# Kernel tuning notes

Measured on AMD Instinct MI355X. Metric: run time of the kernel, lower is better.

## Reference

```python
import jax, jax.numpy as jnp
import numpy as np

# Dimensions (match init_kwargs / input_specs)
NF, NLOC, NALL = 1, 1024, 2048
N_DIM, E_DIM, A_DIM = 128, 16, 64
NNEI, A_SEL, AXIS = 120, 20, 4

act = jax.nn.silu


def _lin(key, i, o):
    k1, k2 = jax.random.split(key)
    w = jax.random.normal(k1, (i, o), jnp.float32) / np.float32(np.sqrt(i))
    b = jax.random.normal(k2, (o,), jnp.float32) * 0.01
    return w, b


def setup_inputs() -> dict:
    key = jax.random.key(0)
    ks = jax.random.split(key, 16)
    d = {}
    d["node_ebd_ext"] = jax.random.normal(ks[0], (NF, NALL, N_DIM), jnp.float32)
    d["edge_ebd"] = jax.random.normal(ks[1], (NF, NLOC, NNEI, E_DIM), jnp.float32)
    d["h2"] = jax.random.normal(ks[2], (NF, NLOC, NNEI, 3), jnp.float32)
    d["angle_ebd"] = jax.random.normal(ks[3], (NF, NLOC, A_SEL, A_SEL, A_DIM), jnp.float32)
    d["sw"] = jax.random.uniform(ks[4], (NF, NLOC, NNEI), jnp.float32)
    d["a_sw"] = jax.random.uniform(ks[5], (NF, NLOC, A_SEL), jnp.float32)
    d["nlist"] = jax.random.randint(ks[6], (NF, NLOC, NNEI), 0, NALL)
    d["nlist_mask"] = jnp.ones((NF, NLOC, NNEI), bool)
    d["a_nlist_mask"] = jnp.ones((NF, NLOC, A_SEL), bool)
    edge_info_dim = 2 * N_DIM + E_DIM          # 272
    angle_dim = A_DIM + N_DIM + 2 * E_DIM      # 224 (a_compress_rate == 0)
    d["w_node_self"], d["b_node_self"] = _lin(ks[7], N_DIM, N_DIM)
    d["w_node_sym"], d["b_node_sym"] = _lin(ks[8], (N_DIM + E_DIM) * AXIS, N_DIM)
    d["w_node_edge"], d["b_node_edge"] = _lin(ks[9], edge_info_dim, N_DIM)
    d["w_edge_self"], d["b_edge_self"] = _lin(ks[10], edge_info_dim, E_DIM)
    d["w_ea1"], d["b_ea1"] = _lin(ks[11], angle_dim, E_DIM)
    d["w_ea2"], d["b_ea2"] = _lin(ks[12], E_DIM, E_DIM)
    d["w_angle_self"], d["b_angle_self"] = _lin(ks[13], angle_dim, A_DIM)
    # res_residual update style: one learnable residual scale per update branch,
    # init 'const' with update_residual = 0.1
    d["n_res"] = jnp.full((3, N_DIM), 0.1, jnp.float32)  # self, sym, edge-message
    d["e_res"] = jnp.full((2, E_DIM), 0.1, jnp.float32)  # self, angle-message
    d["a_res"] = jnp.full((1, A_DIM), 0.1, jnp.float32)  # self
    return d


def _forward(node_ebd_ext, edge_ebd, h2, angle_ebd, sw, a_sw,
             w_node_self, b_node_self, w_node_sym, b_node_sym,
             w_node_edge, b_node_edge, w_edge_self, b_edge_self,
             w_ea1, b_ea1, w_ea2, b_ea2, w_angle_self, b_angle_self,
             n_res, e_res, a_res, nlist, nlist_mask, a_nlist_mask):
    nf, nall, n_dim = node_ebd_ext.shape
    _, nloc, nnei, e_dim = edge_ebd.shape
    a_sel = angle_ebd.shape[2]
    node_ebd = node_ebd_ext[:, :nloc]

    # gather neighbor node embeddings: nf x nloc x nnei x n_dim
    nei_node = jax.vmap(lambda tbl, idx: tbl[idx])(node_ebd_ext, nlist)
    nei_node = jnp.where(nlist_mask[..., None], nei_node, 0.0)

    # 1) node self update
    node_self_update = act(node_ebd @ w_node_self + b_node_self)

    # 2) node symmetrization update (grrg over both edge and neighbor-node features)
    wgt = (sw * nlist_mask)[..., None]

    def sym(ebd):
        e = ebd * wgt
        hg = jnp.einsum('flni,flnd->flid', h2, e) / np.float32(nnei)  # f,l,3,d
        grrg = jnp.einsum('flid,flia->flda', hg, hg[..., :AXIS]) / np.float32(3.0)
        return grrg.reshape(nf, nloc, -1)

    node_sym_in = jnp.concatenate([sym(nei_node), sym(edge_ebd)], axis=-1)
    node_sym_update = act(node_sym_in @ w_node_sym + b_node_sym)

    # 3) edge info = [node_i, node_j, edge_ij]
    node_i = jnp.broadcast_to(node_ebd[:, :, None, :], (nf, nloc, nnei, n_dim))
    edge_info = jnp.concatenate([node_i, nei_node, edge_ebd], axis=-1)

    # 3a) node <- edge message (sw-weighted mean over neighbors)
    node_edge_update = act(edge_info @ w_node_edge + b_node_edge) * sw[..., None]
    node_edge_update = node_edge_update.sum(axis=-2) / np.float32(nnei)

    node_new = (node_ebd + n_res[0] * node_self_update
                + n_res[1] * node_sym_update + n_res[2] * node_edge_update)

    # 4) edge self update
    edge_self_update = act(edge_info @ w_edge_self + b_edge_self)

    # 5) angle branch (a_compress_rate == 0)
    edge_for_angle = jnp.where(a_nlist_mask[..., None], edge_ebd[:, :, :a_sel, :], 0.0)
    node_angle = jnp.broadcast_to(node_ebd[:, :, None, None, :], (nf, nloc, a_sel, a_sel, n_dim))
    e_ik = jnp.broadcast_to(edge_for_angle[:, :, :, None, :], (nf, nloc, a_sel, a_sel, e_dim))
    e_ij = jnp.broadcast_to(edge_for_angle[:, :, None, :, :], (nf, nloc, a_sel, a_sel, e_dim))
    angle_info = jnp.concatenate([angle_ebd, node_angle, e_ik, e_ij], axis=-1)

    # edge <- angle message: sw-weighted reduce over one angle axis
    ea = act(angle_info @ w_ea1 + b_ea1)  # nf,nloc,a_sel,a_sel,e_dim
    weighted = a_sw[:, :, :, None, None] * a_sw[:, :, None, :, None] * ea
    reduced = weighted.sum(axis=-2) / np.float32(np.sqrt(a_sel))  # nf,nloc,a_sel,e_dim
    pad = jnp.zeros((nf, nloc, nnei - a_sel, e_dim), edge_ebd.dtype)
    padded = jnp.concatenate([reduced, pad], axis=2)
    full_mask = jnp.concatenate(
        [a_nlist_mask, jnp.zeros((nf, nloc, nnei - a_sel), bool)], axis=-1)
    # smooth_edge_update = False: keep original edge ebd where angle mask is off
    padded = jnp.where(full_mask[..., None], padded, edge_ebd)
    edge_angle_update = act(padded @ w_ea2 + b_ea2)

    edge_new = edge_ebd + e_res[0] * edge_self_update + e_res[1] * edge_angle_update

    # angle self update
    angle_self_update = act(angle_info @ w_angle_self + b_angle_self)
    angle_new = angle_ebd + a_res[0] * angle_self_update

    return node_new, edge_new, angle_new


def reference(node_ebd_ext, edge_ebd, h2, angle_ebd, sw, a_sw, nlist, nlist_mask,
              a_nlist_mask, w_node_self, b_node_self, w_node_sym, b_node_sym,
              w_node_edge, b_node_edge, w_edge_self, b_edge_self, w_ea1, b_ea1,
              w_ea2, b_ea2, w_angle_self, b_angle_self, n_res, e_res, a_res):
    return _forward(node_ebd_ext, edge_ebd, h2, angle_ebd, sw, a_sw,
                    w_node_self, b_node_self, w_node_sym, b_node_sym,
                    w_node_edge, b_node_edge, w_edge_self, b_edge_self,
                    w_ea1, b_ea1, w_ea2, b_ea2, w_angle_self, b_angle_self,
                    n_res, e_res, a_res, nlist, nlist_mask, a_nlist_mask)
```

## Files before the change

### kernel.cpp

```cpp
#include <hip/hip_runtime.h>
#include <math.h>

#define NLOC 1024
#define NALL 2048
#define NDIM 128
#define EDIM 16
#define ADIM 64
#define NNEI 120
#define ASEL 20


__device__ __forceinline__ float silu(float x) { return x / (1.f + __expf(-x)); }

__device__ __forceinline__ unsigned short f2bf(float f) {
    unsigned int u = __float_as_uint(f);
    u += 0x7fffu + ((u >> 16) & 1u);
    return (unsigned short)(u >> 16);
}

typedef __attribute__((ext_vector_type(8))) short bf16x8;
typedef __attribute__((ext_vector_type(4))) float f32x4;

__global__ __launch_bounds__(256) void k_prep(
    const float* __restrict__ node_ext,
    const float* __restrict__ w_ne, const float* __restrict__ b_ne,
    const float* __restrict__ w_es, const float* __restrict__ b_es,
    const float* __restrict__ w_ea1, const float* __restrict__ b_ea1,
    const float* __restrict__ w_as, const float* __restrict__ b_as,
    float* __restrict__ proj, float* __restrict__ pre_e,
    float* __restrict__ pre_a, unsigned short* __restrict__ wtb)
{
    const int b = blockIdx.x, t = threadIdx.x;
    if (b == 3072) {
        for (int idx = t; idx < 64 * 80; idx += 256) {
            int k = idx / 80, o = idx - k * 80;
            float v = (o < 16) ? w_ea1[k * 16 + o] : w_as[k * 64 + (o - 16)];
            wtb[o * 64 + k] = f2bf(v);
        }
        return;
    }
    __shared__ float x[128];
    const int row = (b < 2048) ? b : (b - 2048);
    if (t < 128) x[t] = node_ext[row * 128 + t];
    __syncthreads();
    if (b < 2048) {
        if (t < 144) {
            float acc = 0.f;
            if (t < 128) {
                for (int k = 0; k < 128; k++) acc += x[k] * w_ne[(128 + k) * 128 + t];
            } else {
                int o = t - 128;
                for (int k = 0; k < 128; k++) acc += x[k] * w_es[(128 + k) * 16 + o];
            }
            proj[b * 144 + t] = acc;
        }
    } else {
        int i = b - 2048;
        if (t < 144) {
            float acc;
            if (t < 128) {
                acc = b_ne[t];
                for (int k = 0; k < 128; k++) acc += x[k] * w_ne[k * 128 + t];
            } else {
                int o = t - 128;
                acc = b_es[o];
                for (int k = 0; k < 128; k++) acc += x[k] * w_es[k * 16 + o];
            }
            pre_e[i * 144 + t] = acc;
        } else if (t < 224) {
            int o = t - 144;
            float acc;
            if (o < 16) {
                acc = b_ea1[o];
                for (int k = 0; k < 128; k++) acc += x[k] * w_ea1[(64 + k) * 16 + o];
            } else {
                int o2 = o - 16;
                acc = b_as[o2];
                for (int k = 0; k < 128; k++) acc += x[k] * w_as[(64 + k) * 64 + o2];
            }
            pre_a[i * 80 + o] = acc;
        }
    }
}

__global__ __launch_bounds__(256) void k_angle(
    const float* __restrict__ angle, const float* __restrict__ edge,
    const float* __restrict__ asw,
    const float* __restrict__ w_ea1, const float* __restrict__ w_as,
    const unsigned short* __restrict__ wtb, const float* __restrict__ pre_a,
    const float* __restrict__ a_res,
    float* __restrict__ out_angle, float* __restrict__ reduced)
{
    const int i = blockIdx.x, t = threadIdx.x;
    const int lane = t & 63, wv = t >> 6;
    const int m = lane & 15, q = lane >> 4;

    __shared__ float eca_s[ASEL * 80], ecb_s[ASEL * 80], edge20_s[ASEL * EDIM];
    __shared__ float asw_s[ASEL], ares_s[ADIM], red_s[ASEL * 16];
    __shared__ unsigned short wt_s[80 * 72];

    for (int idx = t; idx < ASEL * EDIM; idx += 256)
        edge20_s[idx] = edge[(size_t)i * NNEI * EDIM + idx];
    if (t < ASEL) asw_s[t] = asw[i * ASEL + t];
    if (t < ADIM) ares_s[t] = a_res[t];
    for (int idx = t; idx < ASEL * 16; idx += 256) red_s[idx] = 0.f;
    for (int idx = t; idx < 80 * 64; idx += 256) {
        int o = idx >> 6, k = idx & 63;
        wt_s[o * 72 + k] = wtb[idx];
    }
    __syncthreads();

    bf16x8 bfrag[5][2];
    #pragma unroll
    for (int nt = 0; nt < 5; nt++)
        #pragma unroll
        for (int ks = 0; ks < 2; ks++)
            bfrag[nt][ks] = *(const bf16x8*)&wt_s[(nt * 16 + m) * 72 + ks * 32 + q * 8];

    for (int idx = t; idx < 2 * ASEL * 80; idx += 256) {
        int half = idx / 1600, rem = idx - half * 1600;
        int aa = rem / 80, o = rem - aa * 80;
        float acc = (half == 0) ? pre_a[i * 80 + o] : 0.f;
        if (o < 16) {
            const float* w = w_ea1 + (192 + half * 16) * 16 + o;
            #pragma unroll
            for (int k = 0; k < 16; k++) acc += edge20_s[aa * 16 + k] * w[k * 16];
        } else {
            const float* w = w_as + (192 + half * 16) * 64 + (o - 16);
            #pragma unroll
            for (int k = 0; k < 16; k++) acc += edge20_s[aa * 16 + k] * w[k * 64];
        }
        if (half == 0) eca_s[rem] = acc; else ecb_s[rem] = acc;
    }
    __syncthreads();

    for (int mt = wv; mt < 25; mt += 4) {
        const float* Arow = angle + ((size_t)i * 400 + mt * 16 + m) * 64 + q * 8;
        float4 x0 = *(const float4*)(Arow + 0);
        float4 x1 = *(const float4*)(Arow + 4);
        float4 x2 = *(const float4*)(Arow + 32);
        float4 x3 = *(const float4*)(Arow + 36);
        bf16x8 af0, af1;
        af0[0] = (short)f2bf(x0.x); af0[1] = (short)f2bf(x0.y);
        af0[2] = (short)f2bf(x0.z); af0[3] = (short)f2bf(x0.w);
        af0[4] = (short)f2bf(x1.x); af0[5] = (short)f2bf(x1.y);
        af0[6] = (short)f2bf(x1.z); af0[7] = (short)f2bf(x1.w);
        af1[0] = (short)f2bf(x2.x); af1[1] = (short)f2bf(x2.y);
        af1[2] = (short)f2bf(x2.z); af1[3] = (short)f2bf(x2.w);
        af1[4] = (short)f2bf(x3.x); af1[5] = (short)f2bf(x3.y);
        af1[6] = (short)f2bf(x3.z); af1[7] = (short)f2bf(x3.w);

        f32x4 acc[5];
        #pragma unroll
        for (int nt = 0; nt < 5; nt++) {
            acc[nt] = (f32x4){0.f, 0.f, 0.f, 0.f};
            acc[nt] = __builtin_amdgcn_mfma_f32_16x16x32_bf16(af0, bfrag[nt][0], acc[nt], 0, 0, 0);
            acc[nt] = __builtin_amdgcn_mfma_f32_16x16x32_bf16(af1, bfrag[nt][1], acc[nt], 0, 0, 0);
        }

        const int p0 = mt * 16 + q * 4;
        #pragma unroll
        for (int r = 0; r < 4; r++) {
            const int p = p0 + r;
            const int a = p / 20;
            const int bb = p - a * 20;
            {
                const float s = acc[0][r] + eca_s[a * 80 + m] + ecb_s[bb * 80 + m];
                atomicAdd(&red_s[a * 16 + m], asw_s[bb] * silu(s));
            }
            const size_t base = ((size_t)i * 400 + p) * 64;
            #pragma unroll
            for (int nt = 1; nt < 5; nt++) {
                const int o = nt * 16 + m;
                const float s = acc[nt][r] + eca_s[a * 80 + o] + ecb_s[bb * 80 + o];
                const int o2 = o - 16;
                out_angle[base + o2] = angle[base + o2] + ares_s[o2] * silu(s);
            }
        }
    }
    __syncthreads();

    for (int idx = t; idx < ASEL * 16; idx += 256) {
        const int aa = idx >> 4;
        reduced[i * 320 + idx] = red_s[idx] * asw_s[aa] * 0.22360679774997896f;
    }
}

__global__ __launch_bounds__(256) void k_edge(
    const float* __restrict__ edge, const float* __restrict__ sw,
    const int* __restrict__ nlist,
    const float* __restrict__ w_ne, const float* __restrict__ w_es,
    const float* __restrict__ w_ea2, const float* __restrict__ b_ea2,
    const float* __restrict__ e_res,
    const float* __restrict__ proj, const float* __restrict__ pre_e,
    const float* __restrict__ reduced,
    float* __restrict__ neu, float* __restrict__ out_edge)
{
    const int i = blockIdx.x, t = threadIdx.x;
    __shared__ float red_s[320], esu_s[120 * 17], pre_e_s[144];
    __shared__ float wea2_s[256], bea2_s[16], eres_s[32], sw_s[120];
    __shared__ int nl_s[120];

    for (int idx = t; idx < 320; idx += 256) red_s[idx] = reduced[i * 320 + idx];
    if (t < 144) pre_e_s[t] = pre_e[i * 144 + t];
    if (t < 120) { nl_s[t] = nlist[i * 120 + t]; sw_s[t] = sw[i * 120 + t]; }
    if (t < 256) wea2_s[t] = w_ea2[t];
    if (t < 16) bea2_s[t] = b_ea2[t];
    if (t < 32) eres_s[t] = e_res[t];
    __syncthreads();

    if (t < 128) {
        const int o = t;
        float w3c[16];
        #pragma unroll
        for (int k = 0; k < 16; k++) w3c[k] = w_ne[(256 + k) * 128 + o];
        float acc = 0.f;
        for (int j = 0; j < 120; j++) {
            const float* er = edge + ((size_t)i * 120 + j) * 16;
            float s = pre_e_s[o] + proj[(size_t)nl_s[j] * 144 + o];
            float4 e0 = ((const float4*)er)[0], e1 = ((const float4*)er)[1];
            float4 e2 = ((const float4*)er)[2], e3 = ((const float4*)er)[3];
            s += e0.x * w3c[0] + e0.y * w3c[1] + e0.z * w3c[2] + e0.w * w3c[3];
            s += e1.x * w3c[4] + e1.y * w3c[5] + e1.z * w3c[6] + e1.w * w3c[7];
            s += e2.x * w3c[8] + e2.y * w3c[9] + e2.z * w3c[10] + e2.w * w3c[11];
            s += e3.x * w3c[12] + e3.y * w3c[13] + e3.z * w3c[14] + e3.w * w3c[15];
            acc += silu(s) * sw_s[j];
        }
        neu[i * 128 + o] = acc * (1.f / 120.f);
    } else if (t < 248) {
        const int j = t - 128;
        const float* er = edge + ((size_t)i * 120 + j) * 16;
        float e[16];
        #pragma unroll
        for (int k = 0; k < 16; k++) e[k] = er[k];
        const int n = nl_s[j];
        #pragma unroll 1
        for (int oo = 0; oo < 16; oo++) {
            float s = pre_e_s[128 + oo] + proj[(size_t)n * 144 + 128 + oo];
            #pragma unroll
            for (int k = 0; k < 16; k++) s += e[k] * w_es[(256 + k) * 16 + oo];
            esu_s[j * 17 + oo] = silu(s);
        }
    }
    __syncthreads();

    for (int idx = t; idx < 1920; idx += 256) {
        const int j = idx >> 4, o = idx & 15;
        float s = bea2_s[o];
        if (j < 20) {
            #pragma unroll
            for (int k = 0; k < 16; k++) s += red_s[j * 16 + k] * wea2_s[k * 16 + o];
        } else {
            const float* er = edge + ((size_t)i * 120 + j) * 16;
            #pragma unroll
            for (int k = 0; k < 16; k++) s += er[k] * wea2_s[k * 16 + o];
        }
        const float eau = silu(s);
        const float ev = edge[((size_t)i * 120 + j) * 16 + o];
        out_edge[((size_t)i * 120 + j) * 16 + o] =
            ev + eres_s[o] * esu_s[j * 17 + o] + eres_s[16 + o] * eau;
    }
}

__global__ __launch_bounds__(256) void k_node(
    const float* __restrict__ node_ext, const float* __restrict__ edge,
    const float* __restrict__ h2, const float* __restrict__ sw,
    const int* __restrict__ nlist,
    const float* __restrict__ w_ns, const float* __restrict__ b_ns,
    const float* __restrict__ w_sym, const float* __restrict__ b_sym,
    const float* __restrict__ n_res, const float* __restrict__ neu,
    float* __restrict__ out_node)
{
    const int i = blockIdx.x, t = threadIdx.x;
    __shared__ float node_s[128], hjc_s[120 * 4], hgN_s[3 * 128], hgE_s[3 * 16], sym_s[576];
    __shared__ int nl_s[120];

    if (t < 128) node_s[t] = node_ext[i * 128 + t];
    if (t < 120) {
        nl_s[t] = nlist[i * 120 + t];
        const float s = sw[i * 120 + t];
        hjc_s[t * 4 + 0] = h2[((size_t)i * 120 + t) * 3 + 0] * s;
        hjc_s[t * 4 + 1] = h2[((size_t)i * 120 + t) * 3 + 1] * s;
        hjc_s[t * 4 + 2] = h2[((size_t)i * 120 + t) * 3 + 2] * s;
        hjc_s[t * 4 + 3] = 0.f;
    }
    __syncthreads();

    if (t < 128) {
        const int d = t;
        float a0 = 0.f, a1 = 0.f, a2 = 0.f;
        for (int j = 0; j < 120; j++) {
            const float v = node_ext[(size_t)nl_s[j] * 128 + d];
            const float4 hc = *(const float4*)&hjc_s[j * 4];
            a0 += hc.x * v; a1 += hc.y * v; a2 += hc.z * v;
        }
        hgN_s[0 * 128 + d] = a0 * (1.f / 120.f);
        hgN_s[1 * 128 + d] = a1 * (1.f / 120.f);
        hgN_s[2 * 128 + d] = a2 * (1.f / 120.f);
    } else if (t < 144) {
        const int d = t - 128;
        float a0 = 0.f, a1 = 0.f, a2 = 0.f;
        for (int j = 0; j < 120; j++) {
            const float v = edge[((size_t)i * 120 + j) * 16 + d];
            const float4 hc = *(const float4*)&hjc_s[j * 4];
            a0 += hc.x * v; a1 += hc.y * v; a2 += hc.z * v;
        }
        hgE_s[0 * 16 + d] = a0 * (1.f / 120.f);
        hgE_s[1 * 16 + d] = a1 * (1.f / 120.f);
        hgE_s[2 * 16 + d] = a2 * (1.f / 120.f);
    }
    __syncthreads();

    for (int idx = t; idx < 576; idx += 256) {
        if (idx < 512) {
            const int d = idx >> 2, a = idx & 3;
            sym_s[idx] = (hgN_s[d] * hgN_s[a] + hgN_s[128 + d] * hgN_s[128 + a] +
                          hgN_s[256 + d] * hgN_s[256 + a]) * (1.f / 3.f);
        } else {
            const int r = idx - 512, d = r >> 2, a = r & 3;
            sym_s[idx] = (hgE_s[d] * hgE_s[a] + hgE_s[16 + d] * hgE_s[16 + a] +
                          hgE_s[32 + d] * hgE_s[32 + a]) * (1.f / 3.f);
        }
    }
    __syncthreads();

    if (t < 128) {
        const int o = t;
        float s1 = b_ns[o];
        for (int k = 0; k < 128; k++) s1 += node_s[k] * w_ns[k * 128 + o];
        const float nsu = silu(s1);
        float s2 = b_sym[o];
        for (int k = 0; k < 576; k++) s2 += sym_s[k] * w_sym[k * 128 + o];
        const float nsy = silu(s2);
        out_node[i * 128 + o] = node_s[o] + n_res[o] * nsu + n_res[128 + o] * nsy +
                                n_res[256 + o] * neu[i * 128 + o];
    }
}

extern "C" void kernel_launch(void* const* d_in, const int* in_sizes, int n_in,
                              void* d_out, int out_size, void* d_ws, size_t ws_size,
                              hipStream_t stream)
{
    const float* node_ext = (const float*)d_in[0];
    const float* edge     = (const float*)d_in[1];
    const float* h2       = (const float*)d_in[2];
    const float* angle    = (const float*)d_in[3];
    const float* sw       = (const float*)d_in[4];
    const float* asw      = (const float*)d_in[5];
    const int*   nlist    = (const int*)d_in[6];
    const float* w_ns  = (const float*)d_in[9];  const float* b_ns  = (const float*)d_in[10];
    const float* w_sym = (const float*)d_in[11]; const float* b_sym = (const float*)d_in[12];
    const float* w_ne  = (const float*)d_in[13]; const float* b_ne  = (const float*)d_in[14];
    const float* w_es  = (const float*)d_in[15]; const float* b_es  = (const float*)d_in[16];
    const float* w_ea1 = (const float*)d_in[17]; const float* b_ea1 = (const float*)d_in[18];
    const float* w_ea2 = (const float*)d_in[19]; const float* b_ea2 = (const float*)d_in[20];
    const float* w_as  = (const float*)d_in[21]; const float* b_as  = (const float*)d_in[22];
    const float* n_res = (const float*)d_in[23];
    const float* e_res = (const float*)d_in[24];
    const float* a_res = (const float*)d_in[25];

    float* out_node  = (float*)d_out;
    float* out_edge  = out_node + (size_t)NLOC * NDIM;
    float* out_angle = out_edge + (size_t)NLOC * NNEI * EDIM;

    float* ws      = (float*)d_ws;
    float* proj    = ws;
    float* pre_e   = proj + 2048 * 144;
    float* pre_a   = pre_e + 1024 * 144;
    float* reduced = pre_a + 1024 * 80;
    float* neu     = reduced + 1024 * 320;
    unsigned short* wtb = (unsigned short*)(neu + 1024 * 128);

    k_prep<<<dim3(3073), dim3(256), 0, stream>>>(node_ext, w_ne, b_ne, w_es, b_es,
                                                 w_ea1, b_ea1, w_as, b_as,
                                                 proj, pre_e, pre_a, wtb);
    k_angle<<<dim3(1024), dim3(256), 0, stream>>>(angle, edge, asw, w_ea1, w_as,
                                                  wtb, pre_a, a_res, out_angle, reduced);
    k_edge<<<dim3(1024), dim3(256), 0, stream>>>(edge, sw, nlist, w_ne, w_es,
                                                 w_ea2, b_ea2, e_res, proj, pre_e,
                                                 reduced, neu, out_edge);
    k_node<<<dim3(1024), dim3(256), 0, stream>>>(node_ext, edge, h2, sw, nlist,
                                                 w_ns, b_ns, w_sym, b_sym, n_res,
                                                 neu, out_node);
}
```

Baseline: 368.1 us.

## Prefetch global loads and stage edge data in shared memory across kernels

Software-prefetches the next angle tile in k_angle and next gathered proj/node rows in k_edge and k_node, so global latency overlaps compute. Loads B fragments directly from global instead of via LDS, and preloads residual angle values before the MFMAs. Stages edge rows and w_es in shared memory in k_edge, uses a hardware reciprocal in silu, and adds an occupancy hint to k_angle. Costs extra registers and slightly less exact silu division.

```diff
diff --git a/kernel.cpp b/kernel.cpp
--- a/kernel.cpp
+++ b/kernel.cpp
@@ -10,7 +10,9 @@
 #define ASEL 20
 
 
-__device__ __forceinline__ float silu(float x) { return x / (1.f + __expf(-x)); }
+__device__ __forceinline__ float silu(float x) {
+    return x * __builtin_amdgcn_rcpf(1.f + __expf(-x));
+}
 
 __device__ __forceinline__ unsigned short f2bf(float f) {
     unsigned int u = __float_as_uint(f);
@@ -83,7 +85,7 @@
     }
 }
 
-__global__ __launch_bounds__(256) void k_angle(
+__global__ __launch_bounds__(256, 4) void k_angle(
     const float* __restrict__ angle, const float* __restrict__ edge,
     const float* __restrict__ asw,
     const float* __restrict__ w_ea1, const float* __restrict__ w_as,
@@ -97,25 +99,30 @@
 
     __shared__ float eca_s[ASEL * 80], ecb_s[ASEL * 80], edge20_s[ASEL * EDIM];
     __shared__ float asw_s[ASEL], ares_s[ADIM], red_s[ASEL * 16];
-    __shared__ unsigned short wt_s[80 * 72];
+
+    bf16x8 bfrag[5][2];
+    #pragma unroll
+    for (int nt = 0; nt < 5; nt++)
+        #pragma unroll
+        for (int ks = 0; ks < 2; ks++)
+            bfrag[nt][ks] = *(const bf16x8*)&wtb[(nt * 16 + m) * 64 + ks * 32 + q * 8];
 
     for (int idx = t; idx < ASEL * EDIM; idx += 256)
         edge20_s[idx] = edge[(size_t)i * NNEI * EDIM + idx];
     if (t < ASEL) asw_s[t] = asw[i * ASEL + t];
     if (t < ADIM) ares_s[t] = a_res[t];
     for (int idx = t; idx < ASEL * 16; idx += 256) red_s[idx] = 0.f;
-    for (int idx = t; idx < 80 * 64; idx += 256) {
-        int o = idx >> 6, k = idx & 63;
-        wt_s[o * 72 + k] = wtb[idx];
-    }
-    __syncthreads();
-
-    bf16x8 bfrag[5][2];
-    #pragma unroll
-    for (int nt = 0; nt < 5; nt++)
-        #pragma unroll
-        for (int ks = 0; ks < 2; ks++)
-            bfrag[nt][ks] = *(const bf16x8*)&wt_s[(nt * 16 + m) * 72 + ks * 32 + q * 8];
+    __syncthreads();
+
+    int mt = wv;
+    float4 c0, c1, c2, c3;
+    {
+        const float* Arow = angle + ((size_t)i * 400 + mt * 16 + m) * 64 + q * 8;
+        c0 = *(const float4*)(Arow + 0);
+        c1 = *(const float4*)(Arow + 4);
+        c2 = *(const float4*)(Arow + 32);
+        c3 = *(const float4*)(Arow + 36);
+    }
 
     for (int idx = t; idx < 2 * ASEL * 80; idx += 256) {
         int half = idx / 1600, rem = idx - half * 1600;
@@ -134,21 +141,35 @@
     }
     __syncthreads();
 
-    for (int mt = wv; mt < 25; mt += 4) {
-        const float* Arow = angle + ((size_t)i * 400 + mt * 16 + m) * 64 + q * 8;
-        float4 x0 = *(const float4*)(Arow + 0);
-        float4 x1 = *(const float4*)(Arow + 4);
-        float4 x2 = *(const float4*)(Arow + 32);
-        float4 x3 = *(const float4*)(Arow + 36);
+    for (; mt < 25; mt += 4) {
+        const int nmt = mt + 4;
+        float4 n0{}, n1{}, n2{}, n3{};
+        if (nmt < 25) {
+            const float* Arow = angle + ((size_t)i * 400 + nmt * 16 + m) * 64 + q * 8;
+            n0 = *(const float4*)(Arow + 0);
+            n1 = *(const float4*)(Arow + 4);
+            n2 = *(const float4*)(Arow + 32);
+            n3 = *(const float4*)(Arow + 36);
+        }
+
         bf16x8 af0, af1;
-        af0[0] = (short)f2bf(x0.x); af0[1] = (short)f2bf(x0.y);
-        af0[2] = (short)f2bf(x0.z); af0[3] = (short)f2bf(x0.w);
-        af0[4] = (short)f2bf(x1.x); af0[5] = (short)f2bf(x1.y);
-        af0[6] = (short)f2bf(x1.z); af0[7] = (short)f2bf(x1.w);
-        af1[0] = (short)f2bf(x2.x); af1[1] = (short)f2bf(x2.y);
-        af1[2] = (short)f2bf(x2.z); af1[3] = (short)f2bf(x2.w);
-        af1[4] = (short)f2bf(x3.x); af1[5] = (short)f2bf(x3.y);
-        af1[6] = (short)f2bf(x3.z); af1[7] = (short)f2bf(x3.w);
+        af0[0] = (short)f2bf(c0.x); af0[1] = (short)f2bf(c0.y);
+        af0[2] = (short)f2bf(c0.z); af0[3] = (short)f2bf(c0.w);
+        af0[4] = (short)f2bf(c1.x); af0[5] = (short)f2bf(c1.y);
+        af0[6] = (short)f2bf(c1.z); af0[7] = (short)f2bf(c1.w);
+        af1[0] = (short)f2bf(c2.x); af1[1] = (short)f2bf(c2.y);
+        af1[2] = (short)f2bf(c2.z); af1[3] = (short)f2bf(c2.w);
+        af1[4] = (short)f2bf(c3.x); af1[5] = (short)f2bf(c3.y);
+        af1[6] = (short)f2bf(c3.z); af1[7] = (short)f2bf(c3.w);
+
+        const int p0 = mt * 16 + q * 4;
+        float rez[4][4];
+        #pragma unroll
+        for (int r = 0; r < 4; r++) {
+            const float* ar = angle + ((size_t)i * 400 + p0 + r) * 64 + m - 16;
+            #pragma unroll
+            for (int nt = 1; nt < 5; nt++) rez[r][nt - 1] = ar[nt * 16];
+        }
 
         f32x4 acc[5];
         #pragma unroll
@@ -158,7 +179,6 @@
             acc[nt] = __builtin_amdgcn_mfma_f32_16x16x32_bf16(af1, bfrag[nt][1], acc[nt], 0, 0, 0);
         }
 
-        const int p0 = mt * 16 + q * 4;
         #pragma unroll
         for (int r = 0; r < 4; r++) {
             const int p = p0 + r;
@@ -173,10 +193,11 @@
             for (int nt = 1; nt < 5; nt++) {
                 const int o = nt * 16 + m;
                 const float s = acc[nt][r] + eca_s[a * 80 + o] + ecb_s[bb * 80 + o];
-                const int o2 = o - 16;
-                out_angle[base + o2] = angle[base + o2] + ares_s[o2] * silu(s);
+                out_angle[base + o - 16] = rez[r][nt - 1] + ares_s[o - 16] * silu(s);
             }
         }
+
+        c0 = n0; c1 = n1; c2 = n2; c3 = n3;
     }
     __syncthreads();
 
@@ -199,14 +220,22 @@
     const int i = blockIdx.x, t = threadIdx.x;
     __shared__ float red_s[320], esu_s[120 * 17], pre_e_s[144];
     __shared__ float wea2_s[256], bea2_s[16], eres_s[32], sw_s[120];
+    __shared__ float wes_s[256];
+    __shared__ float edge_s[120 * 17];
     __shared__ int nl_s[120];
 
     for (int idx = t; idx < 320; idx += 256) red_s[idx] = reduced[i * 320 + idx];
+    for (int idx = t; idx < 1920; idx += 256) {
+        const int j = idx >> 4, k = idx & 15;
+        edge_s[j * 17 + k] = edge[(size_t)i * 1920 + idx];
+    }
     if (t < 144) pre_e_s[t] = pre_e[i * 144 + t];
     if (t < 120) { nl_s[t] = nlist[i * 120 + t]; sw_s[t] = sw[i * 120 + t]; }
     if (t < 256) wea2_s[t] = w_ea2[t];
     if (t < 16) bea2_s[t] = b_ea2[t];
     if (t < 32) eres_s[t] = e_res[t];
+    if (t >= 128 && t < 128 + 256) ;
+    for (int idx = t; idx < 256; idx += 256) wes_s[idx] = w_es[256 * 16 + idx];
     __syncthreads();
 
     if (t < 128) {
@@ -214,31 +243,35 @@
         float w3c[16];
         #pragma unroll
         for (int k = 0; k < 16; k++) w3c[k] = w_ne[(256 + k) * 128 + o];
+        const float pe = pre_e_s[o];
+        float pj = proj[(size_t)nl_s[0] * 144 + o];
         float acc = 0.f;
         for (int j = 0; j < 120; j++) {
-            const float* er = edge + ((size_t)i * 120 + j) * 16;
-            float s = pre_e_s[o] + proj[(size_t)nl_s[j] * 144 + o];
-            float4 e0 = ((const float4*)er)[0], e1 = ((const float4*)er)[1];
-            float4 e2 = ((const float4*)er)[2], e3 = ((const float4*)er)[3];
-            s += e0.x * w3c[0] + e0.y * w3c[1] + e0.z * w3c[2] + e0.w * w3c[3];
-            s += e1.x * w3c[4] + e1.y * w3c[5] + e1.z * w3c[6] + e1.w * w3c[7];
-            s += e2.x * w3c[8] + e2.y * w3c[9] + e2.z * w3c[10] + e2.w * w3c[11];
-            s += e3.x * w3c[12] + e3.y * w3c[13] + e3.z * w3c[14] + e3.w * w3c[15];
+            float pn = 0.f;
+            if (j + 1 < 120) pn = proj[(size_t)nl_s[j + 1] * 144 + o];
+            const float* er = &edge_s[j * 17];
+            float s = pe + pj;
+            #pragma unroll
+            for (int k = 0; k < 16; k++) s += er[k] * w3c[k];
             acc += silu(s) * sw_s[j];
+            pj = pn;
         }
         neu[i * 128 + o] = acc * (1.f / 120.f);
     } else if (t < 248) {
         const int j = t - 128;
-        const float* er = edge + ((size_t)i * 120 + j) * 16;
+        const int n = nl_s[j];
+        float pv[16];
+        #pragma unroll
+        for (int oo = 0; oo < 16; oo++)
+            pv[oo] = pre_e_s[128 + oo] + proj[(size_t)n * 144 + 128 + oo];
         float e[16];
         #pragma unroll
-        for (int k = 0; k < 16; k++) e[k] = er[k];
-        const int n = nl_s[j];
+        for (int k = 0; k < 16; k++) e[k] = edge_s[j * 17 + k];
         #pragma unroll 1
         for (int oo = 0; oo < 16; oo++) {
-            float s = pre_e_s[128 + oo] + proj[(size_t)n * 144 + 128 + oo];
-            #pragma unroll
-            for (int k = 0; k < 16; k++) s += e[k] * w_es[(256 + k) * 16 + oo];
+            float s = pv[oo];
+            #pragma unroll
+            for (int k = 0; k < 16; k++) s += e[k] * wes_s[k * 16 + oo];
             esu_s[j * 17 + oo] = silu(s);
         }
     }
@@ -251,12 +284,12 @@
             #pragma unroll
             for (int k = 0; k < 16; k++) s += red_s[j * 16 + k] * wea2_s[k * 16 + o];
         } else {
-            const float* er = edge + ((size_t)i * 120 + j) * 16;
+            const float* er = &edge_s[j * 17];
             #pragma unroll
             for (int k = 0; k < 16; k++) s += er[k] * wea2_s[k * 16 + o];
         }
         const float eau = silu(s);
-        const float ev = edge[((size_t)i * 120 + j) * 16 + o];
+        const float ev = edge_s[j * 17 + o];
         out_edge[((size_t)i * 120 + j) * 16 + o] =
             ev + eres_s[o] * esu_s[j * 17 + o] + eres_s[16 + o] * eau;
     }
@@ -289,10 +322,13 @@
     if (t < 128) {
         const int d = t;
         float a0 = 0.f, a1 = 0.f, a2 = 0.f;
+        float v = node_ext[(size_t)nl_s[0] * 128 + d];
         for (int j = 0; j < 120; j++) {
-            const float v = node_ext[(size_t)nl_s[j] * 128 + d];
+            float vn = 0.f;
+            if (j + 1 < 120) vn = node_ext[(size_t)nl_s[j + 1] * 128 + d];
             const float4 hc = *(const float4*)&hjc_s[j * 4];
             a0 += hc.x * v; a1 += hc.y * v; a2 += hc.z * v;
+            v = vn;
         }
         hgN_s[0 * 128 + d] = a0 * (1.f / 120.f);
         hgN_s[1 * 128 + d] = a1 * (1.f / 120.f);
@@ -300,10 +336,13 @@
     } else if (t < 144) {
         const int d = t - 128;
         float a0 = 0.f, a1 = 0.f, a2 = 0.f;
+        float v = edge[((size_t)i * 120 + 0) * 16 + d];
         for (int j = 0; j < 120; j++) {
-            const float v = edge[((size_t)i * 120 + j) * 16 + d];
+            float vn = 0.f;
+            if (j + 1 < 120) vn = edge[((size_t)i * 120 + j + 1) * 16 + d];
             const float4 hc = *(const float4*)&hjc_s[j * 4];
             a0 += hc.x * v; a1 += hc.y * v; a2 += hc.z * v;
+            v = vn;
         }
         hgE_s[0 * 16 + d] = a0 * (1.f / 120.f);
         hgE_s[1 * 16 + d] = a1 * (1.f / 120.f);
```

New measurement: 373.6 us. No clear change (+1.5%).
